# Optimization experiments

Hardware: AMD Instinct MI355X
Metric: run time of the kernel (lower is better)

## Reference

```python
import jax, jax.numpy as jnp
import numpy as np

B, S, H, NH = 8, 4096, 1024, 16
HD = H // NH
EPS_ATTN = 1e-6
EPS_LN = 1e-12


def setup_inputs() -> dict:
    key = jax.random.key(0)
    ks = jax.random.split(key, 10)
    s = 1.0 / np.sqrt(H)
    return {
        "input_tensor": jax.random.normal(ks[0], (B, S, H), dtype=jnp.float32),
        "attention_mask": jnp.zeros((B, S), dtype=jnp.int32),
        "Wq": jax.random.normal(ks[1], (H, H), dtype=jnp.float32) * s,
        "bq": jnp.zeros((H,), dtype=jnp.float32),
        "Wk": jax.random.normal(ks[2], (H, H), dtype=jnp.float32) * s,
        "bk": jnp.zeros((H,), dtype=jnp.float32),
        "Wv": jax.random.normal(ks[3], (H, H), dtype=jnp.float32) * s,
        "bv": jnp.zeros((H,), dtype=jnp.float32),
        "Wd": jax.random.normal(ks[4], (H, H), dtype=jnp.float32) * s,
        "bd": jnp.zeros((H,), dtype=jnp.float32),
        "gamma": jnp.ones((H,), dtype=jnp.float32),
        "beta": jnp.zeros((H,), dtype=jnp.float32),
    }


def reference(input_tensor, attention_mask, Wq, bq, Wk, bk, Wv, bv, Wd, bd, gamma, beta):
    x = input_tensor
    b, s, h = x.shape
    # QKV projections -> [B, S, NH, HD]
    q = (x @ Wq.T + bq).reshape(b, s, NH, HD)
    k = (x @ Wk.T + bk).reshape(b, s, NH, HD)
    v = (x @ Wv.T + bv).reshape(b, s, NH, HD)
    # elu+1 feature map
    q = jax.nn.elu(q) + 1.0
    k = jax.nn.elu(k) + 1.0
    # linear attention: kv state [B, NH, HD_v, HD_k]
    kv = jnp.einsum("nshd,nshm->nhmd", k, v)
    # normalizer: 1 / (q . sum_k)  -> [B, S, NH]
    z = 1.0 / jnp.einsum("nlhd,nhd->nlh", q, k.sum(axis=1) + EPS_ATTN)
    ctx = jnp.einsum("nlhd,nhmd,nlh->nlhm", q, kv, z).reshape(b, s, h)
    # output projection + residual + LayerNorm (dropout is identity in eval)
    hs = ctx @ Wd.T + bd
    hs = hs + x
    mu = hs.mean(axis=-1, keepdims=True)
    var = ((hs - mu) ** 2).mean(axis=-1, keepdims=True)
    out = (hs - mu) / jnp.sqrt(var + EPS_LN) * gamma + beta
    return out
```

## Files before the change

### kernel.cpp

```cpp
#include <hip/hip_runtime.h>
#include <cstdint>
#include <cstddef>

#define BB 8
#define SS 4096
#define HH 1024
#define NHH 16
#define HDD 64
#define MM (BB*SS)
#define KVSPLIT 16

typedef __attribute__((ext_vector_type(8))) short short8_t;
typedef __attribute__((ext_vector_type(4))) float f32x4;

__device__ __forceinline__ float bf2f(short u) {
  unsigned int x = ((unsigned int)(unsigned short)u) << 16;
  return __uint_as_float(x);
}
__device__ __forceinline__ short f2bf(float f) {
  unsigned int u = __float_as_uint(f);
  u += 0x7FFFu + ((u >> 16) & 1u);
  return (short)(u >> 16);
}

__device__ __forceinline__ void gload_lds16(const void* g, void* l) {
  __builtin_amdgcn_global_load_lds(
      (const __attribute__((address_space(1))) void*)g,
      (__attribute__((address_space(3))) void*)l, 16, 0, 0);
}

__global__ void cvt_bf16(const float* __restrict__ in, short* __restrict__ out, int n4) {
  int i = blockIdx.x * blockDim.x + threadIdx.x;
  if (i >= n4) return;
  float4 v = ((const float4*)in)[i];
  short4 o;
  o.x = f2bf(v.x); o.y = f2bf(v.y); o.z = f2bf(v.z); o.w = f2bf(v.w);
  ((short4*)out)[i] = o;
}

__device__ __forceinline__ void gemm128_body(
    const short* __restrict__ A, const short* __restrict__ W,
    const float* __restrict__ bias, short* __restrict__ C,
    int m0, int n0, bool act)
{
  __shared__ __align__(16) short sA[128*32];
  __shared__ __align__(16) short sW[128*32];
  const int t    = threadIdx.x;
  const int lane = t & 63;
  const int wave = t >> 6;
  const int wr = (wave >> 1) * 64;
  const int wc = (wave & 1) * 64;
  const int srow = t >> 2;
  const int scol = (t & 3) * 8;
  const int fr = lane & 15;
  const int fk = (lane >> 4) * 8;

  f32x4 acc[4][4] = {};

  const short* Abase = A + (size_t)(m0 + srow) * HH + scol;
  const short* Wbase = W + (size_t)(n0 + srow) * HH + scol;
  char* lA0 = (char*)sA + t * 16;
  char* lA1 = (char*)sA + 4096 + t * 16;
  char* lW0 = (char*)sW + t * 16;
  char* lW1 = (char*)sW + 4096 + t * 16;

  for (int k0 = 0; k0 < HH; k0 += 32) {
    __syncthreads();
    gload_lds16(Abase + k0,                   lA0);
    gload_lds16(Abase + (size_t)64 * HH + k0, lA1);
    gload_lds16(Wbase + k0,                   lW0);
    gload_lds16(Wbase + (size_t)64 * HH + k0, lW1);
    __syncthreads();

    short8_t af[4], wf[4];
    #pragma unroll
    for (int i = 0; i < 4; i++)
      af[i] = *(const short8_t*)(sA + (wr + i * 16 + fr) * 32 + fk);
    #pragma unroll
    for (int j = 0; j < 4; j++)
      wf[j] = *(const short8_t*)(sW + (wc + j * 16 + fr) * 32 + fk);
    #pragma unroll
    for (int i = 0; i < 4; i++) {
      #pragma unroll
      for (int j = 0; j < 4; j++) {
        acc[i][j] = __builtin_amdgcn_mfma_f32_16x16x32_bf16(af[i], wf[j], acc[i][j], 0, 0, 0);
      }
    }
  }

  const int cr = (lane >> 4) * 4;
  const int cc = lane & 15;
  #pragma unroll
  for (int j = 0; j < 4; j++) {
    const int col = n0 + wc + j * 16 + cc;
    const float bv = bias[col];
    #pragma unroll
    for (int i = 0; i < 4; i++) {
      #pragma unroll
      for (int r = 0; r < 4; r++) {
        const int row = m0 + wr + i * 16 + cr + r;
        float v = acc[i][j][r] + bv;
        if (act) v = (v > 0.f) ? (v + 1.f) : __expf(v);
        C[(size_t)row * HH + col] = f2bf(v);
      }
    }
  }
}

__global__ __launch_bounds__(256, 2) void qkv_gemm(
    const short* __restrict__ xb,
    const short* __restrict__ Wqb, const short* __restrict__ Wkb, const short* __restrict__ Wvb,
    const float* __restrict__ bq, const float* __restrict__ bk, const float* __restrict__ bv,
    short* __restrict__ Qo, short* __restrict__ Ko, short* __restrict__ Vo)
{
  const int which = blockIdx.x >> 3;
  const int n0 = (blockIdx.x & 7) * 128;
  const int m0 = blockIdx.y * 128;
  const short* W  = (which == 0) ? Wqb : (which == 1) ? Wkb : Wvb;
  const float* bs = (which == 0) ? bq  : (which == 1) ? bk  : bv;
  short* C        = (which == 0) ? Qo  : (which == 1) ? Ko  : Vo;
  gemm128_body(xb, W, bs, C, m0, n0, which < 2);
}

__global__ __launch_bounds__(256, 2) void dproj_gemm(
    const short* __restrict__ A, const short* __restrict__ W,
    const float* __restrict__ bias, short* __restrict__ C)
{
  gemm128_body(A, W, bias, C, blockIdx.y * 128, blockIdx.x * 128, false);
}

__global__ __launch_bounds__(256) void kv_part_kernel(
    const short* __restrict__ K_, const short* __restrict__ V_,
    float* __restrict__ kvpart, float* __restrict__ kspart)
{
  __shared__ __align__(16) float sK[32 * 64];
  __shared__ __align__(16) float sV[32 * 64];
  const int h = blockIdx.x, b = blockIdx.y, sp = blockIdx.z;
  const int t = threadIdx.x;
  const int m = t & 63;
  const int dg = (t >> 6) * 16;
  const int lrow = t >> 3;
  const int lcol = (t & 7) * 8;
  const int SC = SS / KVSPLIT;
  float acc[16] = {};
  float ks = 0.f;
  const size_t base = ((size_t)b * SS + (size_t)sp * SC) * HH + (size_t)h * HDD;
  const short* Kp = K_ + base + (size_t)lrow * HH + lcol;
  const short* Vp = V_ + base + (size_t)lrow * HH + lcol;

  for (int sc = 0; sc < SC; sc += 32) {
    short8_t k8 = *(const short8_t*)(Kp + (size_t)sc * HH);
    short8_t v8 = *(const short8_t*)(Vp + (size_t)sc * HH);
    __syncthreads();
    #pragma unroll
    for (int j = 0; j < 8; j++) {
      sK[lrow * 64 + lcol + j] = bf2f(k8[j]);
      sV[lrow * 64 + lcol + j] = bf2f(v8[j]);
    }
    __syncthreads();
    if (t < 64) {
      #pragma unroll
      for (int ss = 0; ss < 32; ss++) ks += sK[ss * 64 + t];
    }
    #pragma unroll 4
    for (int ss = 0; ss < 32; ss++) {
      const float vm = sV[ss * 64 + m];
      const float* kr = sK + ss * 64 + dg;
      #pragma unroll
      for (int j = 0; j < 16; j++) acc[j] += kr[j] * vm;
    }
  }

  const int bh = b * NHH + h;
  float* kvp = kvpart + (size_t)(bh * KVSPLIT + sp) * 4096 + m * 64 + dg;
  #pragma unroll
  for (int j = 0; j < 16; j += 4) {
    f32x4 o;
    o[0] = acc[j]; o[1] = acc[j+1]; o[2] = acc[j+2]; o[3] = acc[j+3];
    *(f32x4*)(kvp + j) = o;
  }
  if (t < 64) kspart[(bh * KVSPLIT + sp) * 64 + t] = ks;
}

__global__ __launch_bounds__(256) void kv_reduce_kernel(
    const float* __restrict__ kvpart, const float* __restrict__ kspart,
    short* __restrict__ kvbf, float* __restrict__ ksum)
{
  const int bh = blockIdx.x;
  const int t = threadIdx.x;
  const float* src = kvpart + (size_t)bh * KVSPLIT * 4096;
  #pragma unroll
  for (int i = 0; i < 4; i++) {
    const int idx = t + i * 256;
    f32x4 s = {};
    #pragma unroll 4
    for (int p = 0; p < KVSPLIT; p++)
      s += ((const f32x4*)(src + (size_t)p * 4096))[idx];
    short4 o;
    o.x = f2bf(s[0]); o.y = f2bf(s[1]); o.z = f2bf(s[2]); o.w = f2bf(s[3]);
    ((short4*)(kvbf + (size_t)bh * 4096))[idx] = o;
  }
  if (t < 64) {
    float s = 0.f;
    #pragma unroll
    for (int p = 0; p < KVSPLIT; p++) s += kspart[(bh * KVSPLIT + p) * 64 + t];
    ksum[bh * 64 + t] = s + 1e-6f;
  }
}

__global__ __launch_bounds__(256) void ctx_mfma(
    const short* __restrict__ Q, const short* __restrict__ kvbf,
    const float* __restrict__ ksum, short* __restrict__ ctx)
{
  __shared__ __align__(16) short sB[64 * 72];
  __shared__ float sks[64];
  __shared__ float sz[256];
  const int b = blockIdx.z, h = blockIdx.y;
  const int t = threadIdx.x;
  const int lane = t & 63, wave = t >> 6;
  const int s0 = blockIdx.x * 256;
  const int bh = b * NHH + h;

  {
    const short8_t* src = (const short8_t*)(kvbf + (size_t)bh * 4096);
    const int m = t >> 2, c = (t & 3) * 16;
    short8_t v0 = src[t * 2], v1 = src[t * 2 + 1];
    *(short8_t*)(sB + m * 72 + c)     = v0;
    *(short8_t*)(sB + m * 72 + c + 8) = v1;
  }
  if (t < 64) sks[t] = ksum[bh * 64 + t];
  __syncthreads();

  {
    const short* qp = Q + (size_t)(b * SS + s0 + t) * HH + h * HDD;
    float zden = 0.f;
    #pragma unroll
    for (int i = 0; i < 8; i++) {
      short8_t q8 = *(const short8_t*)(qp + i * 8);
      #pragma unroll
      for (int j = 0; j < 8; j++) zden += bf2f(q8[j]) * sks[i * 8 + j];
    }
    sz[t] = 1.f / zden;
  }
  __syncthreads();

  const int fr = lane & 15, fk = (lane >> 4) * 8;
  const int wrow = wave * 64;
  f32x4 acc[4][4] = {};
  const short* qbase = Q + (size_t)(b * SS + s0 + wrow + fr) * HH + h * HDD + fk;
  #pragma unroll
  for (int k0 = 0; k0 < 64; k0 += 32) {
    short8_t af[4], wf[4];
    #pragma unroll
    for (int i = 0; i < 4; i++)
      af[i] = *(const short8_t*)(qbase + (size_t)(i * 16) * HH + k0);
    #pragma unroll
    for (int j = 0; j < 4; j++)
      wf[j] = *(const short8_t*)(sB + (j * 16 + fr) * 72 + fk + k0);
    #pragma unroll
    for (int i = 0; i < 4; i++) {
      #pragma unroll
      for (int j = 0; j < 4; j++) {
        acc[i][j] = __builtin_amdgcn_mfma_f32_16x16x32_bf16(af[i], wf[j], acc[i][j], 0, 0, 0);
      }
    }
  }

  const int cr = (lane >> 4) * 4, cc = lane & 15;
  short* cp = ctx + ((size_t)(b * SS + s0)) * HH + h * HDD;
  #pragma unroll
  for (int j = 0; j < 4; j++) {
    const int col = j * 16 + cc;
    #pragma unroll
    for (int i = 0; i < 4; i++) {
      #pragma unroll
      for (int r = 0; r < 4; r++) {
        const int row = wrow + i * 16 + cr + r;
        cp[(size_t)row * HH + col] = f2bf(acc[i][j][r] * sz[row]);
      }
    }
  }
}

__global__ __launch_bounds__(256) void ln_kernel(
    const short* __restrict__ P, const float* __restrict__ x,
    const float* __restrict__ gamma, const float* __restrict__ beta,
    float* __restrict__ out)
{
  const int row = blockIdx.x;
  const int t = threadIdx.x;
  const short* pr = P + (size_t)row * HH;
  const float* xr = x + (size_t)row * HH;
  short4 p4 = ((const short4*)pr)[t];
  float4 x4 = ((const float4*)xr)[t];
  float h0 = bf2f(p4.x) + x4.x;
  float h1 = bf2f(p4.y) + x4.y;
  float h2 = bf2f(p4.z) + x4.z;
  float h3 = bf2f(p4.w) + x4.w;
  float s1 = h0 + h1 + h2 + h3;
  float s2 = h0*h0 + h1*h1 + h2*h2 + h3*h3;
  #pragma unroll
  for (int o = 32; o > 0; o >>= 1) {
    s1 += __shfl_xor(s1, o);
    s2 += __shfl_xor(s2, o);
  }
  __shared__ float red[8];
  const int wv = t >> 6, ln = t & 63;
  if (ln == 0) { red[wv] = s1; red[4 + wv] = s2; }
  __syncthreads();
  const float S1 = red[0] + red[1] + red[2] + red[3];
  const float S2 = red[4] + red[5] + red[6] + red[7];
  const float mu  = S1 * (1.f / HH);
  const float var = S2 * (1.f / HH) - mu * mu;
  const float inv = rsqrtf(var + 1e-12f);
  float4 g4 = ((const float4*)gamma)[t];
  float4 b4 = ((const float4*)beta)[t];
  float4 o4;
  o4.x = (h0 - mu) * inv * g4.x + b4.x;
  o4.y = (h1 - mu) * inv * g4.y + b4.y;
  o4.z = (h2 - mu) * inv * g4.z + b4.z;
  o4.w = (h3 - mu) * inv * g4.w + b4.w;
  ((float4*)(out + (size_t)row * HH))[t] = o4;
}

extern "C" void kernel_launch(void* const* d_in, const int* in_sizes, int n_in,
                              void* d_out, int out_size, void* d_ws, size_t ws_size,
                              hipStream_t stream)
{
  const float* x     = (const float*)d_in[0];
  const float* Wq    = (const float*)d_in[2];
  const float* bq    = (const float*)d_in[3];
  const float* Wk    = (const float*)d_in[4];
  const float* bk    = (const float*)d_in[5];
  const float* Wv    = (const float*)d_in[6];
  const float* bv    = (const float*)d_in[7];
  const float* Wd    = (const float*)d_in[8];
  const float* bd    = (const float*)d_in[9];
  const float* gamma = (const float*)d_in[10];
  const float* beta  = (const float*)d_in[11];
  float* out = (float*)d_out;

  char* ws = (char*)d_ws;
  const size_t MB64 = 67108864;
  short* xb  = (short*)(ws + 0 * MB64);
  short* Qb  = (short*)(ws + 1 * MB64);
  short* Kb  = (short*)(ws + 2 * MB64);
  short* Vb  = (short*)(ws + 3 * MB64);
  short* Cb  = (short*)(ws + 4 * MB64);
  short* Wqb = (short*)(ws + 5 * MB64 + 0 * 2097152);
  short* Wkb = (short*)(ws + 5 * MB64 + 1 * 2097152);
  short* Wvb = (short*)(ws + 5 * MB64 + 2 * 2097152);
  short* Wdb = (short*)(ws + 5 * MB64 + 3 * 2097152);
  short* kvbf= (short*)(ws + 5 * MB64 + 4 * 2097152);
  float* ksb = (float*)(ws + 5 * MB64 + 5 * 2097152);
  float* kvpart = (float*)(ws + 4 * MB64);
  float* kspart = kvpart + (size_t)128 * KVSPLIT * 4096;
  short* Pb  = Qb;

  cvt_bf16<<<(MM * HH / 4) / 256, 256, 0, stream>>>(x,  xb,  MM * HH / 4);
  cvt_bf16<<<(HH * HH / 4) / 256, 256, 0, stream>>>(Wq, Wqb, HH * HH / 4);
  cvt_bf16<<<(HH * HH / 4) / 256, 256, 0, stream>>>(Wk, Wkb, HH * HH / 4);
  cvt_bf16<<<(HH * HH / 4) / 256, 256, 0, stream>>>(Wv, Wvb, HH * HH / 4);
  cvt_bf16<<<(HH * HH / 4) / 256, 256, 0, stream>>>(Wd, Wdb, HH * HH / 4);

  qkv_gemm<<<dim3(24, MM / 128), 256, 0, stream>>>(xb, Wqb, Wkb, Wvb, bq, bk, bv, Qb, Kb, Vb);

  kv_part_kernel<<<dim3(NHH, BB, KVSPLIT), 256, 0, stream>>>(Kb, Vb, kvpart, kspart);
  kv_reduce_kernel<<<BB * NHH, 256, 0, stream>>>(kvpart, kspart, kvbf, ksb);
  ctx_mfma<<<dim3(SS / 256, NHH, BB), 256, 0, stream>>>(Qb, kvbf, ksb, Cb);

  dproj_gemm<<<dim3(HH / 128, MM / 128), 256, 0, stream>>>(Cb, Wdb, bd, Pb);
  ln_kernel<<<MM, 256, 0, stream>>>(Pb, x, gamma, beta, out);
}
```

Baseline: 778.8 us.

## Rewrite projection GEMMs with 256x128 tiles, triple-buffered swizzled LDS pipeline

Replaces the 128x128, BK=32, two-barrier-per-step GEMM body with a 512-thread 256x128 tile, BK=64 kernel. A three-stage LDS ring is filled by direct global-to-LDS loads two k-tiles ahead, with an XOR swizzle against bank conflicts, explicit vmcnt waits and setprio around the MFMA bursts. The epilogue stages bf16 results through LDS so global stores are coalesced 16-byte rows. The goal is to hide global load latency and raise MFMA utilisation in the QKV and output projections. In exchange it uses much more LDS per block (about 144 KB), which may limit occupancy, and relies on fragile hand-written barrier and wait-count logic.

```diff
diff --git a/kernel.cpp b/kernel.cpp
--- a/kernel.cpp
+++ b/kernel.cpp
@@ -10,6 +10,11 @@
 #define MM (BB*SS)
 #define KVSPLIT 16
 
+#define BMt 256
+#define BNt 128
+#define BKt 64
+#define NTt (HH/BKt)
+
 typedef __attribute__((ext_vector_type(8))) short short8_t;
 typedef __attribute__((ext_vector_type(4))) float f32x4;
 
@@ -38,95 +43,146 @@
   ((short4*)out)[i] = o;
 }
 
-__device__ __forceinline__ void gemm128_body(
+__device__ __forceinline__ void gemm256_body(
     const short* __restrict__ A, const short* __restrict__ W,
     const float* __restrict__ bias, short* __restrict__ C,
     int m0, int n0, bool act)
 {
-  __shared__ __align__(16) short sA[128*32];
-  __shared__ __align__(16) short sW[128*32];
-  const int t    = threadIdx.x;
-  const int lane = t & 63;
-  const int wave = t >> 6;
-  const int wr = (wave >> 1) * 64;
-  const int wc = (wave & 1) * 64;
-  const int srow = t >> 2;
-  const int scol = (t & 3) * 8;
-  const int fr = lane & 15;
-  const int fk = (lane >> 4) * 8;
+  __shared__ __align__(16) short sA[3 * BMt * BKt];
+  __shared__ __align__(16) short sB[3 * BNt * BKt];
+
+  const int tid  = threadIdx.x;
+  const int lane = tid & 63;
+  const int wm   = (tid >> 6) >> 1;
+  const int wn   = (tid >> 6) & 1;
+  const int fr   = lane & 15;
+  const int fg   = lane >> 4;
+
+  const int urow  = tid >> 3;
+  const int uslot = tid & 7;
+  const short* Asrc = A + (size_t)(m0 + urow) * HH + ((uslot ^ (urow & 7)) << 3);
+  const short* Bsrc = W + (size_t)(n0 + urow) * HH + ((uslot ^ (urow & 7)) << 3);
+  char* Adst = (char*)sA + tid * 16;
+  char* Bdst = (char*)sB + tid * 16;
+
+#define STG_A(b, kt, u) gload_lds16(Asrc + (size_t)(u) * 64 * HH + (kt) * 64, Adst + (b) * 32768 + (u) * 8192)
+#define STG_B(b, kt, u) gload_lds16(Bsrc + (size_t)(u) * 64 * HH + (kt) * 64, Bdst + (b) * 16384 + (u) * 8192)
+
+  const int swz0 = (( fg)     ^ (fr & 7)) << 4;
+  const int swz1 = ((4 + fg)  ^ (fr & 7)) << 4;
+  const char* Abase = (const char*)sA + (wm * 64 + fr) * 128;
+  const char* Bbase = (const char*)sB + (wn * 64 + fr) * 128;
 
   f32x4 acc[4][4] = {};
 
-  const short* Abase = A + (size_t)(m0 + srow) * HH + scol;
-  const short* Wbase = W + (size_t)(n0 + srow) * HH + scol;
-  char* lA0 = (char*)sA + t * 16;
-  char* lA1 = (char*)sA + 4096 + t * 16;
-  char* lW0 = (char*)sW + t * 16;
-  char* lW1 = (char*)sW + 4096 + t * 16;
-
-  for (int k0 = 0; k0 < HH; k0 += 32) {
-    __syncthreads();
-    gload_lds16(Abase + k0,                   lA0);
-    gload_lds16(Abase + (size_t)64 * HH + k0, lA1);
-    gload_lds16(Wbase + k0,                   lW0);
-    gload_lds16(Wbase + (size_t)64 * HH + k0, lW1);
-    __syncthreads();
-
-    short8_t af[4], wf[4];
-    #pragma unroll
-    for (int i = 0; i < 4; i++)
-      af[i] = *(const short8_t*)(sA + (wr + i * 16 + fr) * 32 + fk);
-    #pragma unroll
-    for (int j = 0; j < 4; j++)
-      wf[j] = *(const short8_t*)(sW + (wc + j * 16 + fr) * 32 + fk);
+  STG_A(0, 0, 0); STG_A(0, 0, 1); STG_A(0, 0, 2); STG_A(0, 0, 3);
+  STG_B(0, 0, 0); STG_B(0, 0, 1);
+  STG_A(1, 1, 0); STG_A(1, 1, 1); STG_A(1, 1, 2); STG_A(1, 1, 3);
+  STG_B(1, 1, 0); STG_B(1, 1, 1);
+  asm volatile("s_waitcnt vmcnt(6)" ::: "memory");
+  __builtin_amdgcn_s_barrier();
+
+  int buf = 0;
+  for (int t = 0; t < NTt; ++t) {
+    const int nb   = (buf >= 1) ? buf - 1 : 2;
+    const int aoff = buf * 32768;
+    const int boff = buf * 16384;
+    const bool pf  = (t + 2 < NTt);
+
+    if (pf) { STG_A(nb, t + 2, 0); STG_A(nb, t + 2, 1); STG_B(nb, t + 2, 0); }
+    {
+      short8_t af[4], bfr[4];
+      #pragma unroll
+      for (int i = 0; i < 4; i++) af[i]  = *(const short8_t*)(Abase + aoff + i * 2048 + swz0);
+      #pragma unroll
+      for (int j = 0; j < 4; j++) bfr[j] = *(const short8_t*)(Bbase + boff + j * 2048 + swz0);
+      __builtin_amdgcn_s_barrier();
+      __builtin_amdgcn_s_setprio(1);
+      #pragma unroll
+      for (int i = 0; i < 4; i++) {
+        #pragma unroll
+        for (int j = 0; j < 4; j++)
+          acc[i][j] = __builtin_amdgcn_mfma_f32_16x16x32_bf16(af[i], bfr[j], acc[i][j], 0, 0, 0);
+      }
+      __builtin_amdgcn_s_setprio(0);
+      __builtin_amdgcn_s_barrier();
+    }
+
+    if (pf) { STG_A(nb, t + 2, 2); STG_A(nb, t + 2, 3); STG_B(nb, t + 2, 1); }
+    {
+      short8_t af[4], bfr[4];
+      #pragma unroll
+      for (int i = 0; i < 4; i++) af[i]  = *(const short8_t*)(Abase + aoff + i * 2048 + swz1);
+      #pragma unroll
+      for (int j = 0; j < 4; j++) bfr[j] = *(const short8_t*)(Bbase + boff + j * 2048 + swz1);
+      __builtin_amdgcn_s_barrier();
+      __builtin_amdgcn_s_setprio(1);
+      #pragma unroll
+      for (int i = 0; i < 4; i++) {
+        #pragma unroll
+        for (int j = 0; j < 4; j++)
+          acc[i][j] = __builtin_amdgcn_mfma_f32_16x16x32_bf16(af[i], bfr[j], acc[i][j], 0, 0, 0);
+      }
+      __builtin_amdgcn_s_setprio(0);
+      if (pf) asm volatile("s_waitcnt vmcnt(6)" ::: "memory");
+      else    asm volatile("s_waitcnt vmcnt(0)" ::: "memory");
+      __builtin_amdgcn_s_barrier();
+    }
+    buf = (buf == 2) ? 0 : buf + 1;
+  }
+#undef STG_A
+#undef STG_B
+
+  short* sC = sA;
+  const int cr = fg * 4;
+  float bvj[4];
+  #pragma unroll
+  for (int j = 0; j < 4; j++) bvj[j] = bias[n0 + wn * 64 + j * 16 + fr];
+  #pragma unroll
+  for (int j = 0; j < 4; j++) {
+    const int col = wn * 64 + j * 16 + fr;
     #pragma unroll
     for (int i = 0; i < 4; i++) {
-      #pragma unroll
-      for (int j = 0; j < 4; j++) {
-        acc[i][j] = __builtin_amdgcn_mfma_f32_16x16x32_bf16(af[i], wf[j], acc[i][j], 0, 0, 0);
+      const int row = wm * 64 + i * 16 + cr;
+      #pragma unroll
+      for (int r = 0; r < 4; r++) {
+        float v = acc[i][j][r] + bvj[j];
+        if (act) v = (v > 0.f) ? (v + 1.f) : __expf(v);
+        sC[(row + r) * 136 + col] = f2bf(v);
       }
     }
   }
-
-  const int cr = (lane >> 4) * 4;
-  const int cc = lane & 15;
-  #pragma unroll
-  for (int j = 0; j < 4; j++) {
-    const int col = n0 + wc + j * 16 + cc;
-    const float bv = bias[col];
-    #pragma unroll
-    for (int i = 0; i < 4; i++) {
-      #pragma unroll
-      for (int r = 0; r < 4; r++) {
-        const int row = m0 + wr + i * 16 + cr + r;
-        float v = acc[i][j][r] + bv;
-        if (act) v = (v > 0.f) ? (v + 1.f) : __expf(v);
-        C[(size_t)row * HH + col] = f2bf(v);
-      }
-    }
-  }
-}
-
-__global__ __launch_bounds__(256, 2) void qkv_gemm(
+  __builtin_amdgcn_s_barrier();
+  const int orow = tid >> 4;
+  const int oc8  = (tid & 15) << 3;
+  #pragma unroll
+  for (int p = 0; p < 8; p++) {
+    const int row = p * 32 + orow;
+    *(short8_t*)(C + (size_t)(m0 + row) * HH + n0 + oc8) =
+        *(const short8_t*)(sC + row * 136 + oc8);
+  }
+}
+
+__global__ __launch_bounds__(512, 2) void qkv_gemm(
     const short* __restrict__ xb,
     const short* __restrict__ Wqb, const short* __restrict__ Wkb, const short* __restrict__ Wvb,
     const float* __restrict__ bq, const float* __restrict__ bk, const float* __restrict__ bv,
     short* __restrict__ Qo, short* __restrict__ Ko, short* __restrict__ Vo)
 {
   const int which = blockIdx.x >> 3;
-  const int n0 = (blockIdx.x & 7) * 128;
-  const int m0 = blockIdx.y * 128;
+  const int n0 = (blockIdx.x & 7) * BNt;
+  const int m0 = blockIdx.y * BMt;
   const short* W  = (which == 0) ? Wqb : (which == 1) ? Wkb : Wvb;
   const float* bs = (which == 0) ? bq  : (which == 1) ? bk  : bv;
   short* C        = (which == 0) ? Qo  : (which == 1) ? Ko  : Vo;
-  gemm128_body(xb, W, bs, C, m0, n0, which < 2);
-}
-
-__global__ __launch_bounds__(256, 2) void dproj_gemm(
+  gemm256_body(xb, W, bs, C, m0, n0, which < 2);
+}
+
+__global__ __launch_bounds__(512, 2) void dproj_gemm(
     const short* __restrict__ A, const short* __restrict__ W,
     const float* __restrict__ bias, short* __restrict__ C)
 {
-  gemm128_body(A, W, bias, C, blockIdx.y * 128, blockIdx.x * 128, false);
+  gemm256_body(A, W, bias, C, blockIdx.y * BMt, blockIdx.x * BNt, false);
 }
 
 __global__ __launch_bounds__(256) void kv_part_kernel(
@@ -363,12 +419,12 @@
   cvt_bf16<<<(HH * HH / 4) / 256, 256, 0, stream>>>(Wv, Wvb, HH * HH / 4);
   cvt_bf16<<<(HH * HH / 4) / 256, 256, 0, stream>>>(Wd, Wdb, HH * HH / 4);
 
-  qkv_gemm<<<dim3(24, MM / 128), 256, 0, stream>>>(xb, Wqb, Wkb, Wvb, bq, bk, bv, Qb, Kb, Vb);
+  qkv_gemm<<<dim3(24, MM / BMt), 512, 0, stream>>>(xb, Wqb, Wkb, Wvb, bq, bk, bv, Qb, Kb, Vb);
 
   kv_part_kernel<<<dim3(NHH, BB, KVSPLIT), 256, 0, stream>>>(Kb, Vb, kvpart, kspart);
   kv_reduce_kernel<<<BB * NHH, 256, 0, stream>>>(kvpart, kspart, kvbf, ksb);
   ctx_mfma<<<dim3(SS / 256, NHH, BB), 256, 0, stream>>>(Qb, kvbf, ksb, Cb);
 
-  dproj_gemm<<<dim3(HH / 128, MM / 128), 256, 0, stream>>>(Cb, Wdb, bd, Pb);
+  dproj_gemm<<<dim3(HH / BNt, MM / BMt), 512, 0, stream>>>(Cb, Wdb, bd, Pb);
   ln_kernel<<<MM, 256, 0, stream>>>(Pb, x, gamma, beta, out);
 }
```

New measurement: 941.5 us. +20.9%, slower.
